# Optimization experiments

Hardware: AMD Instinct MI355X
Metric: run time of the kernel (lower is better)

The kernel has to match this reference:

```python
import jax, jax.numpy as jnp
import numpy as np

B, C, W, H = 16, 512, 64, 64
OUT, NH = 512, 8
HD = OUT // NH          # 64
K = 64                  # kernel_size == attended axis length (height)


def setup_inputs() -> dict:
    key = jax.random.key(0)
    k0, k1, k2, k3 = jax.random.split(key, 4)
    s = float(HD) ** -0.5
    return {
        "x": jax.random.normal(k0, (B, C, W, H), jnp.float32),
        "in_proj_weight": jax.random.normal(k1, (2 * OUT, C), jnp.float32) * s,
        "in_proj_bias": jnp.zeros((2 * OUT,), jnp.float32),
        "out_proj_w": jax.random.normal(k2, (OUT, OUT), jnp.float32) * s,
        "out_proj_b": jnp.zeros((OUT,), jnp.float32),
        "relative": jax.random.normal(k3, (2 * HD, 2 * K - 1), jnp.float32) * s,
    }


def reference(x, in_proj_weight, in_proj_bias, out_proj_w, out_proj_b, relative):
    b, c, w, h = x.shape
    hd2 = HD // 2
    # width=False, self-attention path: permute(0,3,2,1) then flat view
    xq = jnp.transpose(x, (0, 3, 2, 1)).reshape(b * w, h, c)
    qkv = xq @ in_proj_weight.T + in_proj_bias
    q, k, v = jnp.split(qkv, [OUT // 2, OUT], axis=2)

    # relative position embeddings gathered into [2*HD, K, K]
    rel_idx = jnp.arange(K)[:, None] - jnp.arange(K)[None, :] + (K - 1)  # key i, query j
    emb = relative[:, rel_idx]                                          # [2*HD, K, K]
    q_emb, k_emb, v_emb = jnp.split(emb, [hd2, HD], axis=0)

    # [bw, heads, ch, pos]
    q = q.reshape(b * w, h, NH, hd2).transpose(0, 2, 3, 1)
    k = k.reshape(b * w, h, NH, hd2).transpose(0, 2, 3, 1)
    v = v.reshape(b * w, h, NH, HD).transpose(0, 2, 3, 1)

    qr = jnp.einsum('bgci,cij->bgij', q, q_emb)
    kr = jnp.einsum('bgci,cij->bgij', k, k_emb).swapaxes(2, 3)
    qk = jnp.einsum('bgci,bgcj->bgij', q, k)
    sim = jax.nn.softmax(qk + qr + kr, axis=3)

    sv = jnp.einsum('bgij,bgcj->bgci', sim, v)     # [bw, NH, HD, h]
    sve = jnp.einsum('bgij,cij->bgci', sim, v_emb)  # [bw, NH, HD, h]
    out = (sv + sve).reshape(b * w, OUT, h).swapaxes(1, 2)  # [bw, h, OUT]
    out = out @ out_proj_w.T + out_proj_b
    # [b, w, h, OUT] -> transpose(2,3) -> permute(0,2,3,1) == transpose(0,3,2,1)
    out = out.reshape(b, w, h, OUT).transpose(0, 3, 2, 1)   # [B, OUT, H, W]
    return out
```

## Files before the change

### kernel.cpp

```cpp
#include <hip/hip_runtime.h>

using u16 = unsigned short;
using u32 = unsigned int;
typedef __attribute__((ext_vector_type(8))) _Float16 h8v;
typedef __attribute__((ext_vector_type(8))) u16 us8;
typedef __attribute__((ext_vector_type(2))) u32 u32x2;
typedef __attribute__((ext_vector_type(4))) float f4v;

__device__ __forceinline__ u16 f2h(float f) {
  _Float16 h = (_Float16)f;
  return __builtin_bit_cast(unsigned short, h);
}
__device__ __forceinline__ _Float16 bits2h(u16 u) {
  return __builtin_bit_cast(_Float16, u);
}

__device__ __forceinline__ f4v mfma16(h8v a, h8v b, f4v c) {
  return __builtin_amdgcn_mfma_f32_16x16x32_f16(a, b, c, 0, 0, 0);
}

__device__ __forceinline__ void gll16(const void* g, void* l) {
  __builtin_amdgcn_global_load_lds(
      (const __attribute__((address_space(1))) void*)g,
      (__attribute__((address_space(3))) void*)l, 16, 0, 0);
}


__global__ __launch_bounds__(256) void k0_setup(
    const float* __restrict__ w1, const float* __restrict__ wout,
    const float* __restrict__ rel, u16* __restrict__ W1b, u16* __restrict__ Woutb,
    u16* __restrict__ EqT, u16* __restrict__ EkT, u16* __restrict__ Evp)
{
  int idx = blockIdx.x * 256 + threadIdx.x;
  if (idx < 524288) {
    W1b[idx] = f2h(w1[idx]);
  } else if (idx < 786432) {
    int k = idx - 524288; Woutb[k] = f2h(wout[k]);
  } else if (idx < 790528) {
    int k = idx - 786432; int t = k >> 5, c = k & 31;
    EqT[k] = (t < 127) ? f2h(rel[c * 127 + t]) : (u16)0;
  } else if (idx < 794624) {
    int k = idx - 790528; int t = k >> 5, c = k & 31;
    EkT[k] = (t < 127) ? f2h(rel[(32 + c) * 127 + t]) : (u16)0;
  } else if (idx < 802816) {
    int k = idx - 794624; int c = k >> 7, t = k & 127;
    Evp[k] = (t < 127) ? f2h(rel[(64 + c) * 127 + t]) : (u16)0;
  }
}

__global__ __launch_bounds__(256) void k0t_transpose(
    const float* __restrict__ x, u16* __restrict__ xT)
{
  const int bid = blockIdx.x;
  const int cc = bid & 7, w = (bid >> 3) & 63, b = bid >> 9;
  const int c0 = cc * 64;
  const int t = threadIdx.x;
  __shared__ float T[64 * 65];

  const float* xb = x + ((size_t)(b * 512 + c0) * 64 + w) * 64;
#pragma unroll
  for (int p = 0; p < 4; p++) {
    int ci = (t >> 4) + p * 16;
    int pos = (t & 15) * 4;
    float4 v = *(const float4*)&xb[(size_t)ci * 4096 + pos];
    T[ci * 65 + pos + 0] = v.x; T[ci * 65 + pos + 1] = v.y;
    T[ci * 65 + pos + 2] = v.z; T[ci * 65 + pos + 3] = v.w;
  }
  __syncthreads();
  size_t Rb = (size_t)b * 4096 + (size_t)w * 64;
#pragma unroll
  for (int p = 0; p < 2; p++) {
    int u = p * 256 + t;
    int h = u >> 3, ch = u & 7;
    us8 o;
#pragma unroll
    for (int e = 0; e < 8; e++) o[e] = f2h(T[(ch * 8 + e) * 65 + h]);
    *(us8*)&xT[(Rb + h) * 512 + c0 + ch * 8] = o;
  }
}

__global__ __launch_bounds__(256, 2) void k1_qkv(
    const u16* __restrict__ xT, const u16* __restrict__ W1b,
    const float* __restrict__ bias, u16* __restrict__ qkv)
{
  __shared__ u16 POOL[40960];
  u16* XL = POOL;
  u16* WD = POOL + 32768;
  const int bid = blockIdx.x;
  const int b = bid >> 6, w = bid & 63;
  const int tid = threadIdx.x;
  const int l = tid & 63, wv = tid >> 6;
  const int lr = l & 15, lg = l >> 4;
  const int osub = (wv & 1) * 64;
  const int rsub = (wv >> 1) * 32;
  const size_t Rbase = (size_t)bid * 64;

#pragma unroll
  for (int i = 0; i < 16; i++) {
    int r = wv * 16 + i;
    gll16(xT + (Rbase + r) * 512 + ((l ^ (r & 7)) << 3), XL + r * 512);
  }

  auto stageB = [&](int ot, int kk, int buf) {
#pragma unroll
    for (int q = 0; q < 2; q++) {
      int slot = q * 256 + tid;
      int o = slot >> 2, c4 = slot & 3;
      gll16(W1b + (size_t)(ot * 128 + o) * 512 + kk * 32 +
                ((c4 ^ ((o >> 1) & 3)) << 3),
            WD + buf * 4096 + slot * 8);
    }
  };

  stageB(0, 0, 0);
  __syncthreads();

  for (int ot = 0; ot < 8; ot++) {
    const int o0 = ot * 128;
    f4v acc[4][2];
#pragma unroll
    for (int mt = 0; mt < 4; mt++)
#pragma unroll
      for (int nt = 0; nt < 2; nt++) acc[mt][nt] = (f4v){0.f, 0.f, 0.f, 0.f};

#pragma unroll
    for (int kk = 0; kk < 16; kk++) {
      int cur = kk & 1;
      if (kk < 15) stageB(ot, kk + 1, cur ^ 1);
      h8v wf[4], xf[2];
#pragma unroll
      for (int mt = 0; mt < 4; mt++) {
        int o = osub + mt * 16 + lr;
        wf[mt] = *(const h8v*)&WD[cur * 4096 + o * 32 +
                                  ((lg ^ ((o >> 1) & 3)) << 3)];
      }
#pragma unroll
      for (int nt = 0; nt < 2; nt++) {
        int r = rsub + nt * 16 + lr;
        int cc = kk * 4 + lg;
        xf[nt] = *(const h8v*)&XL[r * 512 + ((cc ^ (r & 7)) << 3)];
      }
#pragma unroll
      for (int mt = 0; mt < 4; mt++)
#pragma unroll
        for (int nt = 0; nt < 2; nt++)
          acc[mt][nt] = mfma16(wf[mt], xf[nt], acc[mt][nt]);
      __syncthreads();
    }

    u16* Tr = WD;
    float4 bias4[4];
#pragma unroll
    for (int mt = 0; mt < 4; mt++)
      bias4[mt] = *(const float4*)&bias[o0 + osub + mt * 16 + lg * 4];
#pragma unroll
    for (int mt = 0; mt < 4; mt++)
#pragma unroll
      for (int nt = 0; nt < 2; nt++) {
        int r = rsub + nt * 16 + lr;
#pragma unroll
        for (int ep = 0; ep < 2; ep++) {
          int o_ = osub + mt * 16 + lg * 4 + 2 * ep;
          float v0 = acc[mt][nt][2 * ep + 0] + ((const float*)&bias4[mt])[2 * ep + 0];
          float v1 = acc[mt][nt][2 * ep + 1] + ((const float*)&bias4[mt])[2 * ep + 1];
          unsigned pk = (unsigned)f2h(v0) | ((unsigned)f2h(v1) << 16);
          int cc = o_ >> 3;
          int dst = (cc & 8) | ((cc & 7) ^ (r & 7));
          *(unsigned*)&Tr[r * 128 + dst * 8 + (o_ & 7)] = pk;
        }
      }
    __syncthreads();
#pragma unroll
    for (int p = 0; p < 4; p++) {
      int u = p * 256 + tid;
      int r = u >> 4, cc = u & 15;
      int dst = (cc & 8) | ((cc & 7) ^ (r & 7));
      us8 v = *(const us8*)&Tr[r * 128 + dst * 8];
      size_t S = (size_t)(b * 64 + r) * 64 + w;
      *(us8*)&qkv[S * 1024 + o0 + cc * 8] = v;
    }
    __syncthreads();
    if (ot < 7) { stageB(ot + 1, 0, 0); __syncthreads(); }
  }
}

__global__ __launch_bounds__(256) void k2_attn(
    const u16* __restrict__ qkv, const u16* __restrict__ EqT,
    const u16* __restrict__ EkT, const u16* __restrict__ Evp,
    u16* __restrict__ attn)
{
  const int bid = blockIdx.x;
  const int s = bid >> 3, g = bid & 7;
  const int tid = threadIdx.x;
  const int l = tid & 63, wv = tid >> 6;
  const int lr = l & 15, lg = l >> 4;
  const int i0 = wv * 16;
  const u16* base = qkv + (size_t)s * 65536;

  __shared__ __align__(16) u16 POOL[16896];
  u16* QEi = POOL;
  u16* KEj = POOL + 8448;
  u16* Pl  = POOL;
  u16* VTl = POOL + 4096;
  u16* Psh = POOL + 8192;

  us8 vreg0, vreg1;
  {
    int u0 = tid,        j0_ = u0 >> 3, cb0 = u0 & 7;
    int u1 = tid + 256,  j1_ = u1 >> 3, cb1 = u1 & 7;
    vreg0 = *(const us8*)(base + j0_ * 1024 + 512 + g * 64 + cb0 * 8);
    vreg1 = *(const us8*)(base + j1_ * 1024 + 512 + g * 64 + cb1 * 8);
  }

  h8v qf = *(const h8v*)(base + (i0 + lr) * 1024 + g * 32 + lg * 8);
  h8v kf[4];
#pragma unroll
  for (int jt = 0; jt < 4; jt++)
    kf[jt] = *(const h8v*)(base + (jt * 16 + lr) * 1024 + 256 + g * 32 + lg * 8);

  const f4v z4 = {0.f, 0.f, 0.f, 0.f};

#pragma unroll
  for (int tt = 0; tt < 8; tt++) {
    h8v eb = *(const h8v*)(EqT + (tt * 16 + lr) * 32 + lg * 8);
    f4v d = mfma16(eb, qf, z4);
    int tb = tt * 16 + 4 * lg;
    u32x2 pk;
    pk[0] = (u32)f2h(d[0]) | ((u32)f2h(d[1]) << 16);
    pk[1] = (u32)f2h(d[2]) | ((u32)f2h(d[3]) << 16);
    *(u32x2*)&QEi[(i0 + lr) * 132 + tb] = pk;
  }
#pragma unroll
  for (int q = 0; q < 2; q++) {
    int tt = wv * 2 + q;
    h8v ea = *(const h8v*)(EkT + (tt * 16 + lr) * 32 + lg * 8);
#pragma unroll
    for (int jt = 0; jt < 4; jt++) {
      f4v d = mfma16(ea, kf[jt], z4);
      int tb = tt * 16 + 4 * lg;
      u32x2 pk;
      pk[0] = (u32)f2h(d[0]) | ((u32)f2h(d[1]) << 16);
      pk[1] = (u32)f2h(d[2]) | ((u32)f2h(d[3]) << 16);
      *(u32x2*)&KEj[(jt * 16 + lr) * 132 + tb] = pk;
    }
  }
  f4v sc[4];
#pragma unroll
  for (int jt = 0; jt < 4; jt++) sc[jt] = mfma16(kf[jt], qf, z4);

  __syncthreads();

  const int i = i0 + lr;
  float pv[4][4];
  {
    int qbase = i * 133 + 63 - 4 * lg;
    int kbase = 8448 + 4 * lg * 133 + 63 - i;
#pragma unroll
    for (int jt = 0; jt < 4; jt++)
#pragma unroll
      for (int e = 0; e < 4; e++) {
        float qr = (float)bits2h(POOL[qbase - 16 * jt - e]);
        float kr = (float)bits2h(POOL[kbase + 2128 * jt + 133 * e]);
        pv[jt][e] = sc[jt][e] + qr + kr;
      }
  }
  float inv;
  {
    float m = pv[0][0];
#pragma unroll
    for (int jt = 0; jt < 4; jt++)
#pragma unroll
      for (int e = 0; e < 4; e++) m = fmaxf(m, pv[jt][e]);
    m = fmaxf(m, __shfl_xor(m, 16));
    m = fmaxf(m, __shfl_xor(m, 32));
    float t0 = 0.f;
#pragma unroll
    for (int jt = 0; jt < 4; jt++)
#pragma unroll
      for (int e = 0; e < 4; e++) {
        pv[jt][e] = exp2f((pv[jt][e] - m) * 1.4426950408889634f);
        t0 += pv[jt][e];
      }
    t0 += __shfl_xor(t0, 16);
    t0 += __shfl_xor(t0, 32);
    inv = 1.f / t0;
  }
#pragma unroll
  for (int jt = 0; jt < 4; jt++)
#pragma unroll
    for (int e = 0; e < 4; e++) pv[jt][e] *= inv;

  __syncthreads();

#pragma unroll
  for (int jt = 0; jt < 4; jt++) {
    int j0 = jt * 16 + 4 * lg;
    int jc = j0 >> 3;
    u32x2 pk;
    pk[0] = (u32)f2h(pv[jt][0]) | ((u32)f2h(pv[jt][1]) << 16);
    pk[1] = (u32)f2h(pv[jt][2]) | ((u32)f2h(pv[jt][3]) << 16);
    *(u32x2*)&Pl[i * 64 + ((jc ^ (i & 7)) << 3) + (j0 & 7)] = pk;
#pragma unroll
    for (int e = 0; e < 4; e++) {
      int d = i + 63 - (j0 + e);
      int cd = d >> 3;
      Psh[i * 128 + (((cd & 8) | ((cd & 7) ^ (i & 7))) << 3) + (d & 7)] =
          f2h(pv[jt][e]);
    }
  }
  {
    int zi = tid >> 2;
#pragma unroll
    for (int kk = 0; kk < 16; kk++) {
      int k = (tid & 3) * 16 + kk;
      int col = (k < zi) ? k : (k + 64);
      int cd = col >> 3;
      Psh[zi * 128 + (((cd & 8) | ((cd & 7) ^ (zi & 7))) << 3) + (col & 7)] = 0;
    }
    int u0 = tid, j0_ = u0 >> 3, cb0 = u0 & 7;
#pragma unroll
    for (int e = 0; e < 8; e++) {
      int c = cb0 * 8 + e;
      VTl[c * 64 + (((j0_ >> 3) ^ (c & 7)) << 3) + (j0_ & 7)] = (u16)vreg0[e];
    }
    int u1 = tid + 256, j1_ = u1 >> 3, cb1 = u1 & 7;
#pragma unroll
    for (int e = 0; e < 8; e++) {
      int c = cb1 * 8 + e;
      VTl[c * 64 + (((j1_ >> 3) ^ (c & 7)) << 3) + (j1_ & 7)] = (u16)vreg1[e];
    }
  }
  __syncthreads();

  f4v acc[4] = {z4, z4, z4, z4};
  {
#pragma unroll
    for (int kc = 0; kc < 2; kc++) {
      h8v pa = *(const h8v*)&Pl[i * 64 + (((kc * 4 + lg) ^ (i & 7)) << 3)];
#pragma unroll
      for (int ct = 0; ct < 4; ct++) {
        int cA = ct * 16 + lr;
        h8v vb = *(const h8v*)&VTl[cA * 64 + (((kc * 4 + lg) ^ (cA & 7)) << 3)];
        acc[ct] = mfma16(pa, vb, acc[ct]);
      }
    }
#pragma unroll
    for (int tc = 0; tc < 4; tc++) {
      int cd = tc * 4 + lg;
      int cds = (cd & 8) | ((cd & 7) ^ (i & 7));
      h8v pa = *(const h8v*)&Psh[i * 128 + cds * 8];
#pragma unroll
      for (int ct = 0; ct < 4; ct++) {
        h8v eb = *(const h8v*)(Evp + (ct * 16 + lr) * 128 + tc * 32 + lg * 8);
        acc[ct] = mfma16(pa, eb, acc[ct]);
      }
    }
  }
#pragma unroll
  for (int ct = 0; ct < 4; ct++)
#pragma unroll
    for (int r = 0; r < 4; r++) {
      int io = i0 + lg * 4 + r;
      attn[(size_t)(s * 64 + io) * 512 + g * 64 + ct * 16 + lr] = f2h(acc[ct][r]);
    }
}

__global__ __launch_bounds__(512) void k3_oproj(
    const u16* __restrict__ attn, const u16* __restrict__ Woutb,
    const float* __restrict__ ob, float* __restrict__ out)
{
  const int bid = blockIdx.x;
  const int b = bid >> 6, w = bid & 63;
  const int tid = threadIdx.x;
  const int l = tid & 63, wv = tid >> 6;
  const int lr = l & 15, lg = l >> 4;

  __shared__ u16 Bl[2][64 * 64];

  f4v acc[4][4];
#pragma unroll
  for (int a_ = 0; a_ < 4; a_++)
#pragma unroll
    for (int b_ = 0; b_ < 4; b_++) acc[a_][b_] = (f4v){0.f, 0.f, 0.f, 0.f};

  auto stageB = [&](int kk, int buf) {
    int c0 = kk * 64;
    int h_l = wv * 8 + (l >> 3);
    int p = l & 7;
    const u16* src = attn + ((size_t)b * 4096 + (size_t)h_l * 64 + w) * 512 + c0 +
                     ((p ^ (h_l & 7)) << 3);
    gll16(src, &Bl[buf][wv * 512]);
  };

  stageB(0, 0);
  __syncthreads();

  for (int kk = 0; kk < 8; kk++) {
    int cur = kk & 1, nxt = cur ^ 1;
    if (kk < 7) stageB(kk + 1, nxt);
    int c0 = kk * 64;
    h8v af[4][2], bf[4][2];
#pragma unroll
    for (int mt = 0; mt < 4; mt++)
#pragma unroll
      for (int kc = 0; kc < 2; kc++)
        af[mt][kc] = *(const h8v*)(Woutb + (size_t)(wv * 64 + mt * 16 + lr) * 512 +
                                   c0 + kc * 32 + lg * 8);
#pragma unroll
    for (int jt = 0; jt < 4; jt++)
#pragma unroll
      for (int kc = 0; kc < 2; kc++) {
        int h = jt * 16 + lr;
        bf[jt][kc] = *(const h8v*)&Bl[cur][h * 64 + (((kc * 4 + lg) ^ (h & 7)) << 3)];
      }
#pragma unroll
    for (int mt = 0; mt < 4; mt++)
#pragma unroll
      for (int jt = 0; jt < 4; jt++)
#pragma unroll
        for (int kc = 0; kc < 2; kc++)
          acc[mt][jt] = mfma16(af[mt][kc], bf[jt][kc], acc[mt][jt]);
    __syncthreads();
  }

#pragma unroll
  for (int mt = 0; mt < 4; mt++)
#pragma unroll
    for (int jt = 0; jt < 4; jt++)
#pragma unroll
      for (int e = 0; e < 4; e++) {
        int o = wv * 64 + mt * 16 + lg * 4 + e;
        int h = jt * 16 + lr;
        out[(((size_t)b * 512 + o) * 64 + w) * 64 + h] = acc[mt][jt][e] + ob[o];
      }
}

extern "C" void kernel_launch(void* const* d_in, const int* in_sizes, int n_in,
                              void* d_out, int out_size, void* d_ws, size_t ws_size,
                              hipStream_t stream)
{
  (void)in_sizes; (void)n_in; (void)out_size; (void)ws_size;
  const float* x    = (const float*)d_in[0];
  const float* w1   = (const float*)d_in[1];
  const float* b1   = (const float*)d_in[2];
  const float* wout = (const float*)d_in[3];
  const float* bo   = (const float*)d_in[4];
  const float* rel  = (const float*)d_in[5];
  float* out = (float*)d_out;

  char* ws = (char*)d_ws;
  u16* qkv_ws  = (u16*)ws;
  u16* attn_ws = (u16*)(ws + 134217728);
  u16* xT_ws   = attn_ws;
  u16* W1b     = (u16*)(ws + 201326592);
  u16* Woutb   = (u16*)(ws + 202375168);
  u16* EqT     = (u16*)(ws + 202899456);
  u16* EkT     = (u16*)(ws + 202907648);
  u16* Evp     = (u16*)(ws + 202915840);

  k0_setup<<<dim3(3136), dim3(256), 0, stream>>>(w1, wout, rel, W1b, Woutb, EqT, EkT, Evp);
  k0t_transpose<<<dim3(8192), dim3(256), 0, stream>>>(x, xT_ws);
  k1_qkv  <<<dim3(1024), dim3(256), 0, stream>>>(xT_ws, W1b, b1, qkv_ws);
  k2_attn <<<dim3(8192), dim3(256), 0, stream>>>(qkv_ws, EqT, EkT, Evp, attn_ws);
  k3_oproj<<<dim3(1024), dim3(512), 0, stream>>>(attn_ws, Woutb, bo, out);
}
```

Baseline: 341.8 us.

## Fuse input transpose into QKV projection kernel and split attention launch

Removes the separate transpose kernel; the QKV projection kernel now loads fp32 x directly with strided coalesced reads, converts to fp16 and writes the swizzled tile into LDS. This eliminates the intermediate xT buffer write and re-read and one kernel launch. The attention kernel is also split into two half-grid launches via a block offset. The fused load is synchronous, so x read latency is exposed at the start of each QKV block.

Measured after the change: 335.7 us. Within noise of the previous version (-1.8%).

```diff
diff --git a/kernel.cpp b/kernel.cpp
--- a/kernel.cpp
+++ b/kernel.cpp
@@ -48,39 +48,8 @@
   }
 }
 
-__global__ __launch_bounds__(256) void k0t_transpose(
-    const float* __restrict__ x, u16* __restrict__ xT)
-{
-  const int bid = blockIdx.x;
-  const int cc = bid & 7, w = (bid >> 3) & 63, b = bid >> 9;
-  const int c0 = cc * 64;
-  const int t = threadIdx.x;
-  __shared__ float T[64 * 65];
-
-  const float* xb = x + ((size_t)(b * 512 + c0) * 64 + w) * 64;
-#pragma unroll
-  for (int p = 0; p < 4; p++) {
-    int ci = (t >> 4) + p * 16;
-    int pos = (t & 15) * 4;
-    float4 v = *(const float4*)&xb[(size_t)ci * 4096 + pos];
-    T[ci * 65 + pos + 0] = v.x; T[ci * 65 + pos + 1] = v.y;
-    T[ci * 65 + pos + 2] = v.z; T[ci * 65 + pos + 3] = v.w;
-  }
-  __syncthreads();
-  size_t Rb = (size_t)b * 4096 + (size_t)w * 64;
-#pragma unroll
-  for (int p = 0; p < 2; p++) {
-    int u = p * 256 + t;
-    int h = u >> 3, ch = u & 7;
-    us8 o;
-#pragma unroll
-    for (int e = 0; e < 8; e++) o[e] = f2h(T[(ch * 8 + e) * 65 + h]);
-    *(us8*)&xT[(Rb + h) * 512 + c0 + ch * 8] = o;
-  }
-}
-
 __global__ __launch_bounds__(256, 2) void k1_qkv(
-    const u16* __restrict__ xT, const u16* __restrict__ W1b,
+    const float* __restrict__ x, const u16* __restrict__ W1b,
     const float* __restrict__ bias, u16* __restrict__ qkv)
 {
   __shared__ u16 POOL[40960];
@@ -93,13 +62,6 @@
   const int lr = l & 15, lg = l >> 4;
   const int osub = (wv & 1) * 64;
   const int rsub = (wv >> 1) * 32;
-  const size_t Rbase = (size_t)bid * 64;
-
-#pragma unroll
-  for (int i = 0; i < 16; i++) {
-    int r = wv * 16 + i;
-    gll16(xT + (Rbase + r) * 512 + ((l ^ (r & 7)) << 3), XL + r * 512);
-  }
 
   auto stageB = [&](int ot, int kk, int buf) {
 #pragma unroll
@@ -113,6 +75,24 @@
   };
 
   stageB(0, 0, 0);
+
+  {
+    const int r = tid & 63;
+    const int cb = tid >> 6;
+    const float* xb = x + ((size_t)b * 512 * 64 + w) * 64 + r;
+#pragma unroll
+    for (int q = 0; q < 16; q++) {
+      int cc = (q << 2) | cb;
+      float v[8];
+#pragma unroll
+      for (int e = 0; e < 8; e++)
+        v[e] = xb[(size_t)(cc * 8 + e) * 4096];
+      us8 o;
+#pragma unroll
+      for (int e = 0; e < 8; e++) o[e] = f2h(v[e]);
+      *(us8*)&XL[r * 512 + ((cc ^ (r & 7)) << 3)] = o;
+    }
+  }
   __syncthreads();
 
   for (int ot = 0; ot < 8; ot++) {
@@ -187,9 +167,9 @@
 __global__ __launch_bounds__(256) void k2_attn(
     const u16* __restrict__ qkv, const u16* __restrict__ EqT,
     const u16* __restrict__ EkT, const u16* __restrict__ Evp,
-    u16* __restrict__ attn)
+    u16* __restrict__ attn, int bid0)
 {
-  const int bid = blockIdx.x;
+  const int bid = blockIdx.x + bid0;
   const int s = bid >> 3, g = bid & 7;
   const int tid = threadIdx.x;
   const int l = tid & 63, wv = tid >> 6;
@@ -451,7 +431,6 @@
   char* ws = (char*)d_ws;
   u16* qkv_ws  = (u16*)ws;
   u16* attn_ws = (u16*)(ws + 134217728);
-  u16* xT_ws   = attn_ws;
   u16* W1b     = (u16*)(ws + 201326592);
   u16* Woutb   = (u16*)(ws + 202375168);
   u16* EqT     = (u16*)(ws + 202899456);
@@ -459,8 +438,8 @@
   u16* Evp     = (u16*)(ws + 202915840);
 
   k0_setup<<<dim3(3136), dim3(256), 0, stream>>>(w1, wout, rel, W1b, Woutb, EqT, EkT, Evp);
-  k0t_transpose<<<dim3(8192), dim3(256), 0, stream>>>(x, xT_ws);
-  k1_qkv  <<<dim3(1024), dim3(256), 0, stream>>>(xT_ws, W1b, b1, qkv_ws);
-  k2_attn <<<dim3(8192), dim3(256), 0, stream>>>(qkv_ws, EqT, EkT, Evp, attn_ws);
+  k1_qkv  <<<dim3(1024), dim3(256), 0, stream>>>(x, W1b, b1, qkv_ws);
+  k2_attn <<<dim3(4096), dim3(256), 0, stream>>>(qkv_ws, EqT, EkT, Evp, attn_ws, 0);
+  k2_attn <<<dim3(4096), dim3(256), 0, stream>>>(qkv_ws, EqT, EkT, Evp, attn_ws, 4096);
   k3_oproj<<<dim3(1024), dim3(512), 0, stream>>>(attn_ws, Woutb, bo, out);
 }
```
